# Performance work log

Hardware: AMD Instinct MI355X
Metric: run time of the kernel (lower is better)

The kernel has to match this reference:

```python
import jax, jax.numpy as jnp
import numpy as np

B, D, P, IEXT, T, H = 512, 64, 16, 8, 500, 128
DT = 1.0


def setup_inputs() -> dict:
    key = jax.random.key(0)
    ks = jax.random.split(key, 9)
    s = 0.01  # mimics normal(0.01) kernel init
    return {
        "x": jax.random.normal(ks[0], (B, D, T), jnp.float32),
        "p": jax.random.normal(ks[1], (B, P, T), jnp.float32),
        "i_ext": jax.random.normal(ks[2], (B, IEXT, T), jnp.float32),
        "W0": jax.random.normal(ks[3], (D + P, H), jnp.float32) * s,
        "b0": jax.random.normal(ks[4], (H,), jnp.float32) * s,
        "W1": jax.random.normal(ks[5], (H, H), jnp.float32) * s,
        "b1": jax.random.normal(ks[6], (H,), jnp.float32) * s,
        "W2": jax.random.normal(ks[7], (H, D), jnp.float32) * s,
        "b2": jax.random.normal(ks[8], (D,), jnp.float32) * s,
    }


def reference(x, p, i_ext, W0, b0, W1, b1, W2, b2):
    # Simple_MLP with extra_p=True: concat(state, p) -> Dense+tanh x2 -> Dense
    def mlp(z):
        z = jnp.tanh(z @ W0 + b0)
        z = jnp.tanh(z @ W1 + b1)
        return z @ W2 + b2

    def dfun(state, p_t):
        return mlp(jnp.concatenate([state, p_t], axis=-1))  # [B, D]

    # Heun step: predictor + corrector (two MLP evals), dt = 1.0
    def step(c, p_t):
        d1 = dfun(c, p_t)
        xi = c + DT * d1
        d2 = dfun(xi, p_t)
        nx = c + DT * 0.5 * (d1 + d2)
        return nx, c  # carry new state, emit previous state (as in Heun_step)

    x0 = x[..., 0]                    # [B, D] initial state
    p_seq = jnp.moveaxis(p, 2, 0)     # [T, B, P]
    # i_ext is scanned by the original module but never used by Simple_MLP.
    _, ys = jax.lax.scan(step, x0, p_seq)  # ys: [T, B, D]
    return jnp.moveaxis(ys, 0, 2)     # [B, D, T]
```

## Files before the change

kernel.cpp:

```cpp
#include <hip/hip_runtime.h>

namespace {

constexpr int kB = 512, kD = 64, kP = 16, kT = 500, kH = 128;
constexpr int kKZ = 80;
constexpr int kRows = 16;
constexpr int kBlocks = kB / kRows;
constexpr int kThreads = 256;

constexpr int Z0S = 104;
constexpr int HS = 136;
constexpr int YS = 68;

typedef __attribute__((ext_vector_type(8))) short short8;
typedef __attribute__((ext_vector_type(4))) float float4v;

__device__ __forceinline__ float bf2f(unsigned short u) {
  union { unsigned int i; float f; } v;
  v.i = ((unsigned int)u) << 16;
  return v.f;
}
__device__ __forceinline__ unsigned short f2bf(float f) {
  union { float f; unsigned int i; } v;
  v.f = f;
  return (unsigned short)((v.i + 0x7FFFu + ((v.i >> 16) & 1u)) >> 16);
}
__device__ __forceinline__ void split_bf(float x, unsigned short& hi, unsigned short& lo) {
  hi = f2bf(x);
  lo = f2bf(x - bf2f(hi));
}
#if __has_builtin(__builtin_amdgcn_cvt_pk_bf16_f32)
__device__ __forceinline__ unsigned int pk_bf16(float a, float b) {
  auto v = __builtin_amdgcn_cvt_pk_bf16_f32(a, b);
  unsigned int u;
  __builtin_memcpy(&u, &v, 4);
  return u;
}
#else
__device__ __forceinline__ unsigned int pk_bf16(float a, float b) {
  return (unsigned int)f2bf(a) | ((unsigned int)f2bf(b) << 16);
}
#endif
__device__ __forceinline__ unsigned short f2bf1(float x) {
  return (unsigned short)pk_bf16(x, x);
}
__device__ __forceinline__ void split2(float x, unsigned short& hi, unsigned short& lo) {
  unsigned int uh = pk_bf16(x, x);
  float hif;
  { unsigned int tb = uh << 16; __builtin_memcpy(&hif, &tb, 4); }
  hi = (unsigned short)uh;
  lo = (unsigned short)pk_bf16(x - hif, x - hif);
}
__device__ __forceinline__ float fast_tanh(float x) {
  float e = __builtin_amdgcn_exp2f(x * 2.885390081777927f);
  return 1.0f - 2.0f * __builtin_amdgcn_rcpf(e + 1.0f);
}

__global__ __launch_bounds__(kThreads, 1) void node_kernel(
    const float* __restrict__ xg, const float* __restrict__ pg,
    const float* __restrict__ w0g, const float* __restrict__ b0g,
    const float* __restrict__ w1g, const float* __restrict__ b1g,
    const float* __restrict__ w2g, const float* __restrict__ b2g,
    float* __restrict__ outg) {
  __shared__ __align__(16) unsigned short zh[kRows * Z0S];
  __shared__ __align__(16) unsigned short zl[kRows * Z0S];
  __shared__ __align__(16) unsigned short h0h[kRows * HS];
  __shared__ __align__(16) unsigned short h1h[kRows * HS];
  __shared__ __align__(16) float yb[8][kRows * YS];

  const int tid = threadIdx.x;
  const int wv = tid >> 6;
  const int lane = tid & 63;
  const int l15 = lane & 15;
  const int quad = lane >> 4;
  const int brow = blockIdx.x * kRows;
  const int rswz = (quad & 2) ? 2 : 0;
  const int asw = (l15 & 8) ? 2 : 0;

  short8 w0fh[3][2], w0fl[3][2], w1fh[4][2], w1fl[4][2], w2fh[4], w2fl[4];
  {
    const int k0q = quad * 8;
#pragma unroll
    for (int kt = 0; kt < 3; ++kt)
#pragma unroll
      for (int nt = 0; nt < 2; ++nt) {
        short8 vh, vl;
        const int col = wv * 32 + nt * 16 + l15;
#pragma unroll
        for (int j = 0; j < 8; ++j) {
          int k = kt * 32 + k0q + j;
          unsigned short hi = 0, lo = 0;
          if (k < kKZ) split_bf(w0g[k * kH + col], hi, lo);
          vh[j] = (short)hi; vl[j] = (short)lo;
        }
        w0fh[kt][nt] = vh; w0fl[kt][nt] = vl;
      }
#pragma unroll
    for (int kt = 0; kt < 4; ++kt)
#pragma unroll
      for (int nt = 0; nt < 2; ++nt) {
        short8 vh, vl;
        const int col = wv * 32 + nt * 16 + l15;
#pragma unroll
        for (int j = 0; j < 8; ++j) {
          unsigned short hi, lo;
          split_bf(w1g[(kt * 32 + k0q + j) * kH + col], hi, lo);
          vh[j] = (short)hi; vl[j] = (short)lo;
        }
        w1fh[kt][nt] = vh; w1fl[kt][nt] = vl;
      }
#pragma unroll
    for (int kt = 0; kt < 4; ++kt) {
      short8 vh, vl;
      const int col = wv * 16 + l15;
#pragma unroll
      for (int j = 0; j < 8; ++j) {
        unsigned short hi, lo;
        split_bf(w2g[(kt * 32 + k0q + j) * kD + col], hi, lo);
        vh[j] = (short)hi; vl[j] = (short)lo;
      }
      w2fh[kt] = vh; w2fl[kt] = vl;
    }
  }
  float bias0[2], bias1[2];
#pragma unroll
  for (int nt = 0; nt < 2; ++nt) {
    bias0[nt] = b0g[wv * 32 + nt * 16 + l15];
    bias1[nt] = b1g[wv * 32 + nt * 16 + l15];
  }
  const float bias2 = b2g[wv * 16 + l15];
  const int colL2 = wv * 16 + l15;

  float stR[4], d1R[4];
#pragma unroll
  for (int r = 0; r < 4; ++r)
    stR[r] = xg[((size_t)(brow + quad * 4 + r) * kD + colL2) * kT];

  for (int idx = tid; idx < kRows * kD; idx += kThreads) {
    int r = idx >> 6, c = idx & 63;
    float xv = xg[((size_t)(brow + r) * kD + c) * kT];
    unsigned short hi, lo;
    split_bf(xv, hi, lo);
    int off = r * Z0S + ((((c >> 3) ^ ((r & 8) ? 2 : 0)) << 3) | (c & 7));
    zh[off] = hi;
    zl[off] = lo;
  }
  for (int idx = tid; idx < kRows * 40; idx += kThreads) {
    int r = idx / 40, c = idx % 40;
    zh[r * Z0S + kD + c] = 0;
    zl[r * Z0S + kD + c] = 0;
  }
  const int prow = tid >> 4, ppp = tid & 15;
  const size_t pbase = ((size_t)(brow + prow) * kP + ppp) * kT;
  const int poff = prow * Z0S + ((((8 + (ppp >> 3)) ^ ((prow & 8) ? 2 : 0)) << 3) | (ppp & 7));
  float pv = pg[pbase];
  __syncthreads();

  for (int t = 0; t < kT; ++t) {
    {
      unsigned short hi, lo;
      split2(pv, hi, lo);
      zh[poff] = hi;
      zl[poff] = lo;
    }
    __syncthreads();

    float pvn = 0.0f;
    if (t + 1 < kT) pvn = pg[pbase + t + 1];

    if ((t & 7) == 0 && t) {
      const int t0 = t - 8;
#pragma unroll
      for (int q2 = 0; q2 < 4; ++q2) {
        int idx = tid + q2 * kThreads;
        int r = idx >> 6, c = idx & 63;
        float v[8];
#pragma unroll
        for (int s = 0; s < 8; ++s) v[s] = yb[s][r * YS + c];
        float* dst = outg + ((size_t)(brow + r) * kD + c) * kT + t0;
        float4v vlo = {v[0], v[1], v[2], v[3]}, vhi = {v[4], v[5], v[6], v[7]};
        *(float4v*)(dst) = vlo;
        *(float4v*)(dst + 4) = vhi;
      }
    }

#pragma unroll
    for (int ev = 0; ev < 2; ++ev) {
      short8 a0h[3], a0l[3];
#pragma unroll
      for (int kt = 0; kt < 3; ++kt) {
        const int off = l15 * Z0S + (((kt * 4 + quad) ^ asw) << 3);
        a0h[kt] = *(const short8*)&zh[off];
        a0l[kt] = *(const short8*)&zl[off];
      }
#pragma unroll
      for (int nt = 0; nt < 2; ++nt) {
        float4v ahh = {bias0[nt], bias0[nt], bias0[nt], bias0[nt]};
        float4v ahl = {0.f, 0.f, 0.f, 0.f}, alh = {0.f, 0.f, 0.f, 0.f};
#pragma unroll
        for (int kt = 0; kt < 3; ++kt) {
          ahh = __builtin_amdgcn_mfma_f32_16x16x32_bf16(a0h[kt], w0fh[kt][nt], ahh, 0, 0, 0);
          ahl = __builtin_amdgcn_mfma_f32_16x16x32_bf16(a0h[kt], w0fl[kt][nt], ahl, 0, 0, 0);
          alh = __builtin_amdgcn_mfma_f32_16x16x32_bf16(a0l[kt], w0fh[kt][nt], alh, 0, 0, 0);
        }
        float4v ac = ahh + (ahl + alh);
        const int cb = wv * 4 + nt * 2 + (l15 >> 3);
        const int off = (((cb ^ rswz) << 3) | (l15 & 7));
#pragma unroll
        for (int r = 0; r < 4; ++r)
          h0h[(quad * 4 + r) * HS + off] = f2bf1(fast_tanh(ac[r]));
      }
      __syncthreads();
      short8 a1h[4];
#pragma unroll
      for (int kt = 0; kt < 4; ++kt) {
        const int off = l15 * HS + (((kt * 4 + quad) ^ asw) << 3);
        a1h[kt] = *(const short8*)&h0h[off];
      }
#pragma unroll
      for (int nt = 0; nt < 2; ++nt) {
        float4v ahh = {bias1[nt], bias1[nt], bias1[nt], bias1[nt]};
        float4v ahl = {0.f, 0.f, 0.f, 0.f};
#pragma unroll
        for (int kt = 0; kt < 4; ++kt) {
          ahh = __builtin_amdgcn_mfma_f32_16x16x32_bf16(a1h[kt], w1fh[kt][nt], ahh, 0, 0, 0);
          ahl = __builtin_amdgcn_mfma_f32_16x16x32_bf16(a1h[kt], w1fl[kt][nt], ahl, 0, 0, 0);
        }
        float4v ac = ahh + ahl;
        const int cb = wv * 4 + nt * 2 + (l15 >> 3);
        const int off = (((cb ^ rswz) << 3) | (l15 & 7));
#pragma unroll
        for (int r = 0; r < 4; ++r)
          h1h[(quad * 4 + r) * HS + off] = f2bf1(fast_tanh(ac[r]));
      }
      __syncthreads();
      short8 a2h[4];
#pragma unroll
      for (int kt = 0; kt < 4; ++kt) {
        const int off = l15 * HS + (((kt * 4 + quad) ^ asw) << 3);
        a2h[kt] = *(const short8*)&h1h[off];
      }
      float4v ahh = {bias2, bias2, bias2, bias2};
      float4v ahl = {0.f, 0.f, 0.f, 0.f};
#pragma unroll
      for (int kt = 0; kt < 4; ++kt) {
        ahh = __builtin_amdgcn_mfma_f32_16x16x32_bf16(a2h[kt], w2fh[kt], ahh, 0, 0, 0);
        ahl = __builtin_amdgcn_mfma_f32_16x16x32_bf16(a2h[kt], w2fl[kt], ahl, 0, 0, 0);
      }
      float4v ac = ahh + ahl;

      const int zcb = wv * 2 + (l15 >> 3);
      const int zoff = (((zcb ^ rswz) << 3) | (l15 & 7));
      if (ev == 0) {
#pragma unroll
        for (int r = 0; r < 4; ++r) {
          d1R[r] = ac[r];
          float xi = stR[r] + ac[r];
          unsigned short hi, lo;
          split2(xi, hi, lo);
          zh[(quad * 4 + r) * Z0S + zoff] = hi;
          zl[(quad * 4 + r) * Z0S + zoff] = lo;
        }
        __syncthreads();
      } else {
#pragma unroll
        for (int r = 0; r < 4; ++r) {
          float c = stR[r];
          float nx = c + 0.5f * (ac[r] + d1R[r]);
          yb[t & 7][(quad * 4 + r) * YS + colL2] = c;
          stR[r] = nx;
          unsigned short hi, lo;
          split2(nx, hi, lo);
          zh[(quad * 4 + r) * Z0S + zoff] = hi;
          zl[(quad * 4 + r) * Z0S + zoff] = lo;
        }
      }
    }
    pv = pvn;
  }
  __syncthreads();
  {
    const int t0 = (kT / 8) * 8;
#pragma unroll
    for (int q2 = 0; q2 < 4; ++q2) {
      int idx = tid + q2 * kThreads;
      int r = idx >> 6, c = idx & 63;
      float v[4];
#pragma unroll
      for (int s = 0; s < 4; ++s) v[s] = yb[s][r * YS + c];
      float* dst = outg + ((size_t)(brow + r) * kD + c) * kT + t0;
      float4v vv = {v[0], v[1], v[2], v[3]};
      *(float4v*)(dst) = vv;
    }
  }
}

}

extern "C" void kernel_launch(void* const* d_in, const int* in_sizes, int n_in,
                              void* d_out, int out_size, void* d_ws, size_t ws_size,
                              hipStream_t stream) {
  const float* xg = (const float*)d_in[0];
  const float* pg = (const float*)d_in[1];
  const float* w0g = (const float*)d_in[3];
  const float* b0g = (const float*)d_in[4];
  const float* w1g = (const float*)d_in[5];
  const float* b1g = (const float*)d_in[6];
  const float* w2g = (const float*)d_in[7];
  const float* b2g = (const float*)d_in[8];
  float* outg = (float*)d_out;

  hipLaunchKernelGGL(node_kernel, dim3(kBlocks), dim3(kThreads), 0, stream,
                     xg, pg, w0g, b0g, w1g, b1g, w2g, b2g, outg);
}
```

Measured before the change: 1.325 ms.

## Split MLP columns over eight waves and hoist the p-part of layer 0

Doubles the block to 512 threads so each of eight waves computes one 16-column tile of layers 0 and 1 instead of two, which halves per-wave MFMA chains on the serial time-step critical path. The p contribution to layer 0 is computed once per time step and reused for both Heun evaluations. Layer 2 and the state update run only on the first four waves, leaving the others idle there. More waves join every barrier and launch bounds now target two waves per SIMD, which may raise synchronisation cost and register pressure.

```diff
diff --git a/kernel.cpp b/kernel.cpp
--- a/kernel.cpp
+++ b/kernel.cpp
@@ -6,7 +6,7 @@
 constexpr int kKZ = 80;
 constexpr int kRows = 16;
 constexpr int kBlocks = kB / kRows;
-constexpr int kThreads = 256;
+constexpr int kThreads = 512;
 
 constexpr int Z0S = 104;
 constexpr int HS = 136;
@@ -56,7 +56,7 @@
   return 1.0f - 2.0f * __builtin_amdgcn_rcpf(e + 1.0f);
 }
 
-__global__ __launch_bounds__(kThreads, 1) void node_kernel(
+__global__ __launch_bounds__(kThreads, 2) void node_kernel(
     const float* __restrict__ xg, const float* __restrict__ pg,
     const float* __restrict__ w0g, const float* __restrict__ b0g,
     const float* __restrict__ w1g, const float* __restrict__ b1g,
@@ -77,59 +77,60 @@
   const int rswz = (quad & 2) ? 2 : 0;
   const int asw = (l15 & 8) ? 2 : 0;
 
-  short8 w0fh[3][2], w0fl[3][2], w1fh[4][2], w1fl[4][2], w2fh[4], w2fl[4];
+  const int col01 = wv * 16 + l15;
+  const int colL2 = (wv & 3) * 16 + l15;
+
+  short8 w0fh[2], w0fl[2], w0pfh, w0pfl, w1fh[4], w1fl[4], w2fh[4], w2fl[4];
   {
     const int k0q = quad * 8;
 #pragma unroll
-    for (int kt = 0; kt < 3; ++kt)
-#pragma unroll
-      for (int nt = 0; nt < 2; ++nt) {
-        short8 vh, vl;
-        const int col = wv * 32 + nt * 16 + l15;
-#pragma unroll
-        for (int j = 0; j < 8; ++j) {
-          int k = kt * 32 + k0q + j;
-          unsigned short hi = 0, lo = 0;
-          if (k < kKZ) split_bf(w0g[k * kH + col], hi, lo);
-          vh[j] = (short)hi; vl[j] = (short)lo;
-        }
-        w0fh[kt][nt] = vh; w0fl[kt][nt] = vl;
-      }
-#pragma unroll
-    for (int kt = 0; kt < 4; ++kt)
-#pragma unroll
-      for (int nt = 0; nt < 2; ++nt) {
-        short8 vh, vl;
-        const int col = wv * 32 + nt * 16 + l15;
-#pragma unroll
-        for (int j = 0; j < 8; ++j) {
-          unsigned short hi, lo;
-          split_bf(w1g[(kt * 32 + k0q + j) * kH + col], hi, lo);
-          vh[j] = (short)hi; vl[j] = (short)lo;
-        }
-        w1fh[kt][nt] = vh; w1fl[kt][nt] = vl;
-      }
+    for (int kt = 0; kt < 2; ++kt) {
+      short8 vh, vl;
+#pragma unroll
+      for (int j = 0; j < 8; ++j) {
+        unsigned short hi, lo;
+        split_bf(w0g[(kt * 32 + k0q + j) * kH + col01], hi, lo);
+        vh[j] = (short)hi; vl[j] = (short)lo;
+      }
+      w0fh[kt] = vh; w0fl[kt] = vl;
+    }
+    {
+      short8 vh, vl;
+#pragma unroll
+      for (int j = 0; j < 8; ++j) {
+        int k = 64 + k0q + j;
+        unsigned short hi = 0, lo = 0;
+        if (k < kKZ) split_bf(w0g[k * kH + col01], hi, lo);
+        vh[j] = (short)hi; vl[j] = (short)lo;
+      }
+      w0pfh = vh; w0pfl = vl;
+    }
 #pragma unroll
     for (int kt = 0; kt < 4; ++kt) {
       short8 vh, vl;
-      const int col = wv * 16 + l15;
 #pragma unroll
       for (int j = 0; j < 8; ++j) {
         unsigned short hi, lo;
-        split_bf(w2g[(kt * 32 + k0q + j) * kD + col], hi, lo);
+        split_bf(w1g[(kt * 32 + k0q + j) * kH + col01], hi, lo);
         vh[j] = (short)hi; vl[j] = (short)lo;
       }
+      w1fh[kt] = vh; w1fl[kt] = vl;
+    }
+#pragma unroll
+    for (int kt = 0; kt < 4; ++kt) {
+      short8 vh, vl;
+#pragma unroll
+      for (int j = 0; j < 8; ++j) {
+        unsigned short hi, lo;
+        split_bf(w2g[(kt * 32 + k0q + j) * kD + colL2], hi, lo);
+        vh[j] = (short)hi; vl[j] = (short)lo;
+      }
       w2fh[kt] = vh; w2fl[kt] = vl;
     }
   }
-  float bias0[2], bias1[2];
-#pragma unroll
-  for (int nt = 0; nt < 2; ++nt) {
-    bias0[nt] = b0g[wv * 32 + nt * 16 + l15];
-    bias1[nt] = b1g[wv * 32 + nt * 16 + l15];
-  }
-  const float bias2 = b2g[wv * 16 + l15];
-  const int colL2 = wv * 16 + l15;
+  const float bias0 = b0g[col01];
+  const float bias1 = b1g[col01];
+  const float bias2 = b2g[colL2];
 
   float stR[4], d1R[4];
 #pragma unroll
@@ -150,14 +151,14 @@
     zh[r * Z0S + kD + c] = 0;
     zl[r * Z0S + kD + c] = 0;
   }
-  const int prow = tid >> 4, ppp = tid & 15;
+  const int prow = (tid >> 4) & 15, ppp = tid & 15;
   const size_t pbase = ((size_t)(brow + prow) * kP + ppp) * kT;
   const int poff = prow * Z0S + ((((8 + (ppp >> 3)) ^ ((prow & 8) ? 2 : 0)) << 3) | (ppp & 7));
-  float pv = pg[pbase];
+  float pv = (tid < 256) ? pg[pbase] : 0.0f;
   __syncthreads();
 
   for (int t = 0; t < kT; ++t) {
-    {
+    if (tid < 256) {
       unsigned short hi, lo;
       split2(pv, hi, lo);
       zh[poff] = hi;
@@ -166,12 +167,12 @@
     __syncthreads();
 
     float pvn = 0.0f;
-    if (t + 1 < kT) pvn = pg[pbase + t + 1];
+    if (tid < 256 && t + 1 < kT) pvn = pg[pbase + t + 1];
 
     if ((t & 7) == 0 && t) {
       const int t0 = t - 8;
 #pragma unroll
-      for (int q2 = 0; q2 < 4; ++q2) {
+      for (int q2 = 0; q2 < 2; ++q2) {
         int idx = tid + q2 * kThreads;
         int r = idx >> 6, c = idx & 63;
         float v[8];
@@ -184,27 +185,37 @@
       }
     }
 
+    float4v phh, phl, plh;
+    {
+      const int off = l15 * Z0S + (((8 + quad) ^ asw) << 3);
+      short8 aph = *(const short8*)&zh[off];
+      short8 apl = *(const short8*)&zl[off];
+      float4v z4 = {0.f, 0.f, 0.f, 0.f};
+      float4v b4 = {bias0, bias0, bias0, bias0};
+      phh = __builtin_amdgcn_mfma_f32_16x16x32_bf16(aph, w0pfh, b4, 0, 0, 0);
+      phl = __builtin_amdgcn_mfma_f32_16x16x32_bf16(aph, w0pfl, z4, 0, 0, 0);
+      plh = __builtin_amdgcn_mfma_f32_16x16x32_bf16(apl, w0pfh, z4, 0, 0, 0);
+    }
+
 #pragma unroll
     for (int ev = 0; ev < 2; ++ev) {
-      short8 a0h[3], a0l[3];
-#pragma unroll
-      for (int kt = 0; kt < 3; ++kt) {
+      short8 a0h[2], a0l[2];
+#pragma unroll
+      for (int kt = 0; kt < 2; ++kt) {
         const int off = l15 * Z0S + (((kt * 4 + quad) ^ asw) << 3);
         a0h[kt] = *(const short8*)&zh[off];
         a0l[kt] = *(const short8*)&zl[off];
       }
-#pragma unroll
-      for (int nt = 0; nt < 2; ++nt) {
-        float4v ahh = {bias0[nt], bias0[nt], bias0[nt], bias0[nt]};
-        float4v ahl = {0.f, 0.f, 0.f, 0.f}, alh = {0.f, 0.f, 0.f, 0.f};
-#pragma unroll
-        for (int kt = 0; kt < 3; ++kt) {
-          ahh = __builtin_amdgcn_mfma_f32_16x16x32_bf16(a0h[kt], w0fh[kt][nt], ahh, 0, 0, 0);
-          ahl = __builtin_amdgcn_mfma_f32_16x16x32_bf16(a0h[kt], w0fl[kt][nt], ahl, 0, 0, 0);
-          alh = __builtin_amdgcn_mfma_f32_16x16x32_bf16(a0l[kt], w0fh[kt][nt], alh, 0, 0, 0);
+      {
+        float4v ahh = phh, ahl = phl, alh = plh;
+#pragma unroll
+        for (int kt = 0; kt < 2; ++kt) {
+          ahh = __builtin_amdgcn_mfma_f32_16x16x32_bf16(a0h[kt], w0fh[kt], ahh, 0, 0, 0);
+          ahl = __builtin_amdgcn_mfma_f32_16x16x32_bf16(a0h[kt], w0fl[kt], ahl, 0, 0, 0);
+          alh = __builtin_amdgcn_mfma_f32_16x16x32_bf16(a0l[kt], w0fh[kt], alh, 0, 0, 0);
         }
         float4v ac = ahh + (ahl + alh);
-        const int cb = wv * 4 + nt * 2 + (l15 >> 3);
+        const int cb = wv * 2 + (l15 >> 3);
         const int off = (((cb ^ rswz) << 3) | (l15 & 7));
 #pragma unroll
         for (int r = 0; r < 4; ++r)
@@ -217,62 +228,68 @@
         const int off = l15 * HS + (((kt * 4 + quad) ^ asw) << 3);
         a1h[kt] = *(const short8*)&h0h[off];
       }
-#pragma unroll
-      for (int nt = 0; nt < 2; ++nt) {
-        float4v ahh = {bias1[nt], bias1[nt], bias1[nt], bias1[nt]};
+      {
+        float4v ahh = {bias1, bias1, bias1, bias1};
         float4v ahl = {0.f, 0.f, 0.f, 0.f};
 #pragma unroll
         for (int kt = 0; kt < 4; ++kt) {
-          ahh = __builtin_amdgcn_mfma_f32_16x16x32_bf16(a1h[kt], w1fh[kt][nt], ahh, 0, 0, 0);
-          ahl = __builtin_amdgcn_mfma_f32_16x16x32_bf16(a1h[kt], w1fl[kt][nt], ahl, 0, 0, 0);
+          ahh = __builtin_amdgcn_mfma_f32_16x16x32_bf16(a1h[kt], w1fh[kt], ahh, 0, 0, 0);
+          ahl = __builtin_amdgcn_mfma_f32_16x16x32_bf16(a1h[kt], w1fl[kt], ahl, 0, 0, 0);
         }
         float4v ac = ahh + ahl;
-        const int cb = wv * 4 + nt * 2 + (l15 >> 3);
+        const int cb = wv * 2 + (l15 >> 3);
         const int off = (((cb ^ rswz) << 3) | (l15 & 7));
 #pragma unroll
         for (int r = 0; r < 4; ++r)
           h1h[(quad * 4 + r) * HS + off] = f2bf1(fast_tanh(ac[r]));
       }
       __syncthreads();
-      short8 a2h[4];
-#pragma unroll
-      for (int kt = 0; kt < 4; ++kt) {
-        const int off = l15 * HS + (((kt * 4 + quad) ^ asw) << 3);
-        a2h[kt] = *(const short8*)&h1h[off];
-      }
-      float4v ahh = {bias2, bias2, bias2, bias2};
-      float4v ahl = {0.f, 0.f, 0.f, 0.f};
-#pragma unroll
-      for (int kt = 0; kt < 4; ++kt) {
-        ahh = __builtin_amdgcn_mfma_f32_16x16x32_bf16(a2h[kt], w2fh[kt], ahh, 0, 0, 0);
-        ahl = __builtin_amdgcn_mfma_f32_16x16x32_bf16(a2h[kt], w2fl[kt], ahl, 0, 0, 0);
-      }
-      float4v ac = ahh + ahl;
-
-      const int zcb = wv * 2 + (l15 >> 3);
+      float4v ac;
+      if (wv < 4) {
+        short8 a2h[4];
+#pragma unroll
+        for (int kt = 0; kt < 4; ++kt) {
+          const int off = l15 * HS + (((kt * 4 + quad) ^ asw) << 3);
+          a2h[kt] = *(const short8*)&h1h[off];
+        }
+        float4v ahh = {bias2, bias2, bias2, bias2};
+        float4v ahl = {0.f, 0.f, 0.f, 0.f};
+#pragma unroll
+        for (int kt = 0; kt < 4; ++kt) {
+          ahh = __builtin_amdgcn_mfma_f32_16x16x32_bf16(a2h[kt], w2fh[kt], ahh, 0, 0, 0);
+          ahl = __builtin_amdgcn_mfma_f32_16x16x32_bf16(a2h[kt], w2fl[kt], ahl, 0, 0, 0);
+        }
+        ac = ahh + ahl;
+      }
+
+      const int zcb = (wv & 3) * 2 + (l15 >> 3);
       const int zoff = (((zcb ^ rswz) << 3) | (l15 & 7));
       if (ev == 0) {
-#pragma unroll
-        for (int r = 0; r < 4; ++r) {
-          d1R[r] = ac[r];
-          float xi = stR[r] + ac[r];
-          unsigned short hi, lo;
-          split2(xi, hi, lo);
-          zh[(quad * 4 + r) * Z0S + zoff] = hi;
-          zl[(quad * 4 + r) * Z0S + zoff] = lo;
+        if (wv < 4) {
+#pragma unroll
+          for (int r = 0; r < 4; ++r) {
+            d1R[r] = ac[r];
+            float xi = stR[r] + ac[r];
+            unsigned short hi, lo;
+            split2(xi, hi, lo);
+            zh[(quad * 4 + r) * Z0S + zoff] = hi;
+            zl[(quad * 4 + r) * Z0S + zoff] = lo;
+          }
         }
         __syncthreads();
       } else {
-#pragma unroll
-        for (int r = 0; r < 4; ++r) {
-          float c = stR[r];
-          float nx = c + 0.5f * (ac[r] + d1R[r]);
-          yb[t & 7][(quad * 4 + r) * YS + colL2] = c;
-          stR[r] = nx;
-          unsigned short hi, lo;
-          split2(nx, hi, lo);
-          zh[(quad * 4 + r) * Z0S + zoff] = hi;
-          zl[(quad * 4 + r) * Z0S + zoff] = lo;
+        if (wv < 4) {
+#pragma unroll
+          for (int r = 0; r < 4; ++r) {
+            float c = stR[r];
+            float nx = c + 0.5f * (ac[r] + d1R[r]);
+            yb[t & 7][(quad * 4 + r) * YS + colL2] = c;
+            stR[r] = nx;
+            unsigned short hi, lo;
+            split2(nx, hi, lo);
+            zh[(quad * 4 + r) * Z0S + zoff] = hi;
+            zl[(quad * 4 + r) * Z0S + zoff] = lo;
+          }
         }
       }
     }
@@ -282,7 +299,7 @@
   {
     const int t0 = (kT / 8) * 8;
 #pragma unroll
-    for (int q2 = 0; q2 < 4; ++q2) {
+    for (int q2 = 0; q2 < 2; ++q2) {
       int idx = tid + q2 * kThreads;
       int r = idx >> 6, c = idx & 63;
       float v[4];
```

Result: faster. 1.211 ms (-8.6%).
